# Optimization experiments

Hardware: AMD Instinct MI355X
Metric: run time of the kernel (lower is better)

The kernel has to match this reference:

```python
import jax, jax.numpy as jnp
import numpy as np


def hard_sigmoid(x):
    # Keras hard_sigmoid: clip(0.2*x + 0.5, 0, 1)
    return jnp.clip(0.2 * x + 0.5, 0.0, 1.0)


def setup_inputs() -> dict:
    key = jax.random.key(0)
    k1, k2, k3 = jax.random.split(key, 3)
    B, H, W, C = 32, 64, 64, 256
    x = jax.random.normal(k1, (B, H, W, C), dtype=jnp.float32)
    # glorot_uniform over (C, W, H): fan_in = W (last-two matmul dims are W x H)
    limit = np.sqrt(6.0 / (W + H)).astype(np.float32)
    Wq = jax.random.uniform(k2, (C, W, H), minval=-limit, maxval=limit, dtype=jnp.float32)
    Wk = jax.random.uniform(k3, (C, W, H), minval=-limit, maxval=limit, dtype=jnp.float32)
    return {"x": x, "Wq": Wq, "Wk": Wk}


def reference(x, Wq, Wk):
    # x: [B, H, W, C] -> [B, C, H, W]
    xt = jnp.transpose(x, (0, 3, 1, 2))
    # projections: [B,C,H,W] @ [C,W,H] (broadcast over B) -> [B,C,H,H]
    q = hard_sigmoid(jnp.einsum('bchw,cwk->bchk', xt, Wq))
    K = jnp.tanh(jnp.einsum('bchw,cwk->bchk', xt, Wk))
    # scores: q @ K^T over last two dims -> [B,C,H,H]
    qk = hard_sigmoid(jnp.einsum('bchk,bcmk->bchm', q, K))
    qk = jax.nn.softmax(qk, axis=-1)
    # output: [B,C,H,W] @ [B,C,W(==H),H] -> [B,C,H,H]
    out = jnp.einsum('bchw,bcwm->bchm', xt, qk)
    # back to channels-last [B,H,W,C]
    return jnp.transpose(out, (0, 2, 3, 1))
```

## Files before the change

### kernel.cpp

```cpp
#include <hip/hip_runtime.h>
#include <hip/hip_bf16.h>


typedef short short8 __attribute__((ext_vector_type(8)));
typedef float floatx4 __attribute__((ext_vector_type(4)));
typedef unsigned int uint;

#define PW 16896
#define BUF1_OFF 8192

__device__ __forceinline__ uint bfr(float f) {
  uint u = __float_as_uint(f);
  return (u + 0x7FFFu + ((u >> 16) & 1u)) >> 16;
}
__device__ __forceinline__ uint pk2(float a, float b) {
  return bfr(a) | (bfr(b) << 16);
}
__device__ __forceinline__ short8 u4s8(uint a, uint b, uint c, uint d) {
  union { uint u[4]; short8 s; } t;
  t.u[0] = a; t.u[1] = b; t.u[2] = c; t.u[3] = d;
  return t.s;
}
__device__ __forceinline__ float hsg(float x) {
  return fminf(fmaxf(0.2f * x + 0.5f, 0.f), 1.f);
}

__global__ __launch_bounds__(256, 2) void fused_attn(
    const float* __restrict__ x, const float* __restrict__ Wq,
    const float* __restrict__ Wk, float* __restrict__ out) {
  __shared__ __align__(16) unsigned char smem[4 * PW];

  const int tid  = threadIdx.x;
  const int lane = tid & 63;
  const int wid  = tid >> 6;
  const int l15  = lane & 15;
  const int quad = lane >> 4;

  const int b  = blockIdx.x & 31;
  const int cg = blockIdx.x >> 5;
  const int c0 = cg << 2;
  const int c  = c0 + wid;

  unsigned char* buf0 = smem + wid * PW;
  unsigned char* buf1 = buf0 + BUF1_OFF;

  {
    const float* xb = x + (size_t)b * 4096 * 256 + c0;
#pragma unroll 4
    for (int it = 0; it < 16; ++it) {
      int hw = it * 256 + tid;
      float4 v = *(const float4*)(xb + (size_t)hw * 256);
      int h = hw >> 6, w = hw & 63;
      uint off = (uint)(h * 128 + (((w >> 3) ^ (h & 7)) << 4) + ((w & 7) << 1));
      float vv[4] = {v.x, v.y, v.z, v.w};
#pragma unroll
      for (int j = 0; j < 4; ++j)
        *(unsigned short*)(smem + j * PW + off) = (unsigned short)bfr(vv[j]);
    }
  }
  __syncthreads();

  short8 xf[4][2];
#pragma unroll
  for (int rt = 0; rt < 4; ++rt) {
    int r = rt * 16 + l15;
#pragma unroll
    for (int ks = 0; ks < 2; ++ks)
      xf[rt][ks] = *(const short8*)(buf0 + r * 128 + ((((ks * 4 + quad) ^ (r & 7))) << 4));
  }

  const floatx4 zero4 = {0.f, 0.f, 0.f, 0.f};
  floatx4 acc[16];

  {
    const float* wp = Wq + (size_t)c * 4096;
#pragma unroll 4
    for (int j = 0; j < 16; ++j) {
      int f4 = j * 64 + lane;
      float4 v = *(const float4*)(wp + (size_t)f4 * 4);
      int w = f4 >> 4, k0 = (f4 & 15) << 2;
      uint2 pk; pk.x = pk2(v.x, v.y); pk.y = pk2(v.z, v.w);
      *(uint2*)(buf1 + w * 136 + k0 * 2) = pk;
    }
  }
#pragma unroll
  for (int i = 0; i < 16; ++i) acc[i] = zero4;
#pragma unroll
  for (int kt = 0; kt < 4; ++kt) {
    short8 af[2];
#pragma unroll
    for (int ks = 0; ks < 2; ++ks) {
      const unsigned short* p = (const unsigned short*)buf1 + (ks * 32 + quad * 8) * 68 + (kt * 16 + l15);
      af[ks] = u4s8((uint)p[0]   | ((uint)p[68]  << 16),
                    (uint)p[136] | ((uint)p[204] << 16),
                    (uint)p[272] | ((uint)p[340] << 16),
                    (uint)p[408] | ((uint)p[476] << 16));
    }
#pragma unroll
    for (int ht = 0; ht < 4; ++ht) {
      acc[kt * 4 + ht] = __builtin_amdgcn_mfma_f32_16x16x32_bf16(af[0], xf[ht][0], acc[kt * 4 + ht], 0, 0, 0);
      acc[kt * 4 + ht] = __builtin_amdgcn_mfma_f32_16x16x32_bf16(af[1], xf[ht][1], acc[kt * 4 + ht], 0, 0, 0);
    }
  }
#pragma unroll
  for (int kt = 0; kt < 4; ++kt)
#pragma unroll
    for (int ht = 0; ht < 4; ++ht) {
      floatx4 a = acc[kt * 4 + ht];
      uint2 pk; pk.x = pk2(hsg(a[0]), hsg(a[1])); pk.y = pk2(hsg(a[2]), hsg(a[3]));
      int h = ht * 16 + l15;
      *(uint2*)(buf0 + h * 128 + ((((kt * 2 + (quad >> 1)) ^ (h & 7))) << 4) + ((quad & 1) << 3)) = pk;
    }

  {
    const float* wp = Wk + (size_t)c * 4096;
#pragma unroll 4
    for (int j = 0; j < 16; ++j) {
      int f4 = j * 64 + lane;
      float4 v = *(const float4*)(wp + (size_t)f4 * 4);
      int w = f4 >> 4, k0 = (f4 & 15) << 2;
      uint2 pk; pk.x = pk2(v.x, v.y); pk.y = pk2(v.z, v.w);
      *(uint2*)(buf1 + w * 136 + k0 * 2) = pk;
    }
  }
#pragma unroll
  for (int i = 0; i < 16; ++i) acc[i] = zero4;
#pragma unroll
  for (int kt = 0; kt < 4; ++kt) {
    short8 af[2];
#pragma unroll
    for (int ks = 0; ks < 2; ++ks) {
      const unsigned short* p = (const unsigned short*)buf1 + (ks * 32 + quad * 8) * 68 + (kt * 16 + l15);
      af[ks] = u4s8((uint)p[0]   | ((uint)p[68]  << 16),
                    (uint)p[136] | ((uint)p[204] << 16),
                    (uint)p[272] | ((uint)p[340] << 16),
                    (uint)p[408] | ((uint)p[476] << 16));
    }
#pragma unroll
    for (int ht = 0; ht < 4; ++ht) {
      acc[kt * 4 + ht] = __builtin_amdgcn_mfma_f32_16x16x32_bf16(af[0], xf[ht][0], acc[kt * 4 + ht], 0, 0, 0);
      acc[kt * 4 + ht] = __builtin_amdgcn_mfma_f32_16x16x32_bf16(af[1], xf[ht][1], acc[kt * 4 + ht], 0, 0, 0);
    }
  }
#pragma unroll
  for (int kt = 0; kt < 4; ++kt)
#pragma unroll
    for (int ht = 0; ht < 4; ++ht) {
      floatx4 a = acc[kt * 4 + ht];
      float kv[4];
#pragma unroll
      for (int i = 0; i < 4; ++i) {
        float t = __expf(2.f * a[i]);
        kv[i] = 1.f - 2.f / (t + 1.f);
      }
      uint2 pk; pk.x = pk2(kv[0], kv[1]); pk.y = pk2(kv[2], kv[3]);
      int m = ht * 16 + l15;
      *(uint2*)(buf1 + m * 128 + ((((kt * 2 + (quad >> 1)) ^ (m & 7))) << 4) + ((quad & 1) << 3)) = pk;
    }

  short8 kf[4][2];
#pragma unroll
  for (int mt = 0; mt < 4; ++mt) {
    int r = mt * 16 + l15;
#pragma unroll
    for (int ks = 0; ks < 2; ++ks)
      kf[mt][ks] = *(const short8*)(buf1 + r * 128 + ((((ks * 4 + quad) ^ (r & 7))) << 4));
  }
#pragma unroll
  for (int i = 0; i < 16; ++i) acc[i] = zero4;
#pragma unroll
  for (int wt = 0; wt < 4; ++wt) {
    int r = wt * 16 + l15;
    short8 qf0 = *(const short8*)(buf0 + r * 128 + (((quad ^ (r & 7))) << 4));
    short8 qf1 = *(const short8*)(buf0 + r * 128 + ((((4 + quad) ^ (r & 7))) << 4));
#pragma unroll
    for (int mt = 0; mt < 4; ++mt) {
      acc[wt * 4 + mt] = __builtin_amdgcn_mfma_f32_16x16x32_bf16(qf0, kf[mt][0], acc[wt * 4 + mt], 0, 0, 0);
      acc[wt * 4 + mt] = __builtin_amdgcn_mfma_f32_16x16x32_bf16(qf1, kf[mt][1], acc[wt * 4 + mt], 0, 0, 0);
    }
  }
#pragma unroll
  for (int i = 0; i < 16; ++i)
#pragma unroll
    for (int j = 0; j < 4; ++j) acc[i][j] = __expf(hsg(acc[i][j]));
  float inv[4][4];
#pragma unroll
  for (int wt = 0; wt < 4; ++wt)
#pragma unroll
    for (int i = 0; i < 4; ++i) {
      float p = acc[wt * 4 + 0][i] + acc[wt * 4 + 1][i] + acc[wt * 4 + 2][i] + acc[wt * 4 + 3][i];
      p += __shfl_xor(p, 1, 16);
      p += __shfl_xor(p, 2, 16);
      p += __shfl_xor(p, 4, 16);
      p += __shfl_xor(p, 8, 16);
      inv[wt][i] = 1.f / p;
    }
#pragma unroll
  for (int wt = 0; wt < 4; ++wt)
#pragma unroll
    for (int mt = 0; mt < 4; ++mt) {
      floatx4 a = acc[wt * 4 + mt];
      uint2 pk;
      pk.x = pk2(a[0] * inv[wt][0], a[1] * inv[wt][1]);
      pk.y = pk2(a[2] * inv[wt][2], a[3] * inv[wt][3]);
      int m = mt * 16 + l15;
      *(uint2*)(buf0 + m * 128 + ((((wt * 2 + (quad >> 1)) ^ (m & 7))) << 4) + ((quad & 1) << 3)) = pk;
    }

#pragma unroll
  for (int i = 0; i < 16; ++i) acc[i] = zero4;
#pragma unroll
  for (int mt = 0; mt < 4; ++mt) {
    int r = mt * 16 + l15;
    short8 sf0 = *(const short8*)(buf0 + r * 128 + (((quad ^ (r & 7))) << 4));
    short8 sf1 = *(const short8*)(buf0 + r * 128 + ((((4 + quad) ^ (r & 7))) << 4));
#pragma unroll
    for (int ht = 0; ht < 4; ++ht) {
      acc[mt * 4 + ht] = __builtin_amdgcn_mfma_f32_16x16x32_bf16(sf0, xf[ht][0], acc[mt * 4 + ht], 0, 0, 0);
      acc[mt * 4 + ht] = __builtin_amdgcn_mfma_f32_16x16x32_bf16(sf1, xf[ht][1], acc[mt * 4 + ht], 0, 0, 0);
    }
  }
#pragma unroll
  for (int mt = 0; mt < 4; ++mt)
#pragma unroll
    for (int ht = 0; ht < 4; ++ht) {
      floatx4 a = acc[mt * 4 + ht];
      uint2 pk; pk.x = pk2(a[0], a[1]); pk.y = pk2(a[2], a[3]);
      int h = ht * 16 + l15;
      *(uint2*)(buf1 + h * 128 + ((((mt * 2 + (quad >> 1)) ^ (h & 7))) << 4) + ((quad & 1) << 3)) = pk;
    }
  __syncthreads();

  const size_t outbase = (size_t)b * 4096 * 256 + c0;
#pragma unroll
  for (int rep = 0; rep < 4; ++rep) {
    int idx = rep * 256 + tid;
    int h = idx >> 4, mq = idx & 15;
    uint loff = (uint)(h * 128 + ((((mq >> 1) ^ (h & 7))) << 4) + ((mq & 1) << 3));
    float vals[4][4];
#pragma unroll
    for (int j = 0; j < 4; ++j) {
      uint2 d = *(const uint2*)(smem + j * PW + BUF1_OFF + loff);
      vals[j][0] = __uint_as_float(d.x << 16);
      vals[j][1] = __uint_as_float(d.x & 0xFFFF0000u);
      vals[j][2] = __uint_as_float(d.y << 16);
      vals[j][3] = __uint_as_float(d.y & 0xFFFF0000u);
    }
    float* op = out + outbase + (size_t)(h * 64 + mq * 4) * 256;
#pragma unroll
    for (int jj = 0; jj < 4; ++jj) {
      float4 v = {vals[0][jj], vals[1][jj], vals[2][jj], vals[3][jj]};
      *(float4*)(op + (size_t)jj * 256) = v;
    }
  }
}

extern "C" void kernel_launch(void* const* d_in, const int* in_sizes, int n_in,
                              void* d_out, int out_size, void* d_ws, size_t ws_size,
                              hipStream_t stream) {
  const float* x  = (const float*)d_in[0];
  const float* Wq = (const float*)d_in[1];
  const float* Wk = (const float*)d_in[2];
  float* o = (float*)d_out;
  fused_attn<<<dim3(2048), dim3(256), 0, stream>>>(x, Wq, Wk, o);
}
```

Measured before the change: 323.7 us.

## Prepack weights in prep kernel, use register lane swaps and hardware bf16 convert

Adds a prep kernel that converts Wq/Wk to bf16 once, already laid out as MFMA A-operand fragments in workspace. The main kernel no longer reloads and transposes the weights per batch block. Q and the softmax scores are rearranged into MFMA operand layout with permlane swaps in registers instead of a round trip through LDS, which shrinks LDS use enough to target 3 blocks per CU. It also switches bf16 rounding to the v_cvt_pk_bf16_f32 instruction, widens the x loads, and wraps MFMA loops in s_setprio. The risks are an extra kernel launch and higher register pressure from holding fragments in registers.

Result: slower. 332.8 us (+2.8%).

```diff
diff --git a/kernel.cpp b/kernel.cpp
--- a/kernel.cpp
+++ b/kernel.cpp
@@ -1,20 +1,14 @@
 #include <hip/hip_runtime.h>
-#include <hip/hip_bf16.h>
 
 
 typedef short short8 __attribute__((ext_vector_type(8)));
 typedef float floatx4 __attribute__((ext_vector_type(4)));
 typedef unsigned int uint;
 
-#define PW 16896
-#define BUF1_OFF 8192
-
-__device__ __forceinline__ uint bfr(float f) {
-  uint u = __float_as_uint(f);
-  return (u + 0x7FFFu + ((u >> 16) & 1u)) >> 16;
-}
-__device__ __forceinline__ uint pk2(float a, float b) {
-  return bfr(a) | (bfr(b) << 16);
+__device__ __forceinline__ uint cvtpk(float a, float b) {
+  uint r;
+  asm("v_cvt_pk_bf16_f32 %0, %1, %2" : "=v"(r) : "v"(a), "v"(b));
+  return r;
 }
 __device__ __forceinline__ short8 u4s8(uint a, uint b, uint c, uint d) {
   union { uint u[4]; short8 s; } t;
@@ -25,10 +19,74 @@
   return fminf(fmaxf(0.2f * x + 0.5f, 0.f), 1.f);
 }
 
-__global__ __launch_bounds__(256, 2) void fused_attn(
-    const float* __restrict__ x, const float* __restrict__ Wq,
-    const float* __restrict__ Wk, float* __restrict__ out) {
-  __shared__ __align__(16) unsigned char smem[4 * PW];
+__device__ __forceinline__ void pl32swap(uint A, uint C, uint& lo, uint& hi, int quad) {
+#if __has_builtin(__builtin_amdgcn_permlane32_swap)
+  auto r = __builtin_amdgcn_permlane32_swap(A, C, false, false);
+  lo = (uint)r[0]; hi = (uint)r[1];
+#else
+  uint sA = __shfl_xor(A, 32), sC = __shfl_xor(C, 32);
+  bool up = quad >= 2;
+  lo = up ? sC : A;
+  hi = up ? C : sA;
+#endif
+}
+__device__ __forceinline__ void pl16swap(uint A, uint C, uint& lo, uint& hi, int quad) {
+#if __has_builtin(__builtin_amdgcn_permlane16_swap)
+  auto r = __builtin_amdgcn_permlane16_swap(A, C, false, false);
+  lo = (uint)r[0]; hi = (uint)r[1];
+#else
+  uint sA = (uint)__builtin_amdgcn_ds_swizzle((int)A, 0x401F);
+  uint sC = (uint)__builtin_amdgcn_ds_swizzle((int)C, 0x401F);
+  bool odd = quad & 1;
+  lo = odd ? sC : A;
+  hi = odd ? C : sA;
+#endif
+}
+__device__ __forceinline__ short8 xchg4(uint A, uint B, uint C, uint D, int quad) {
+  uint Ap, Cp, Bp, Dp, t0, t1, t2, t3;
+  pl32swap(A, C, Ap, Cp, quad);
+  pl32swap(B, D, Bp, Dp, quad);
+  pl16swap(Ap, Cp, t0, t2, quad);
+  pl16swap(Bp, Dp, t1, t3, quad);
+  return u4s8(t0, t1, t2, t3);
+}
+
+__global__ __launch_bounds__(256) void prep_w(const float* __restrict__ Wq,
+                                              const float* __restrict__ Wk,
+                                              unsigned short* __restrict__ ws) {
+  __shared__ __align__(16) unsigned char sm[4 * 8704];
+  const int tid = threadIdx.x, lane = tid & 63, wid = tid >> 6;
+  const int task = blockIdx.x * 4 + wid;
+  const int c = task & 255;
+  const float* wp = ((task >> 8) ? Wk : Wq) + (size_t)c * 4096;
+  unsigned char* buf = sm + wid * 8704;
+  const int l15 = lane & 15, quad = lane >> 4;
+#pragma unroll 4
+  for (int j = 0; j < 16; ++j) {
+    int f4 = j * 64 + lane;
+    float4 v = *(const float4*)(wp + (size_t)f4 * 4);
+    int w = f4 >> 4, k0 = (f4 & 15) << 2;
+    uint2 pk; pk.x = cvtpk(v.x, v.y); pk.y = cvtpk(v.z, v.w);
+    *(uint2*)(buf + w * 136 + k0 * 2) = pk;
+  }
+  unsigned short* dst = ws + (size_t)task * 4096;
+#pragma unroll
+  for (int kt = 0; kt < 4; ++kt)
+#pragma unroll
+    for (int ks = 0; ks < 2; ++ks) {
+      const unsigned short* p = (const unsigned short*)buf + (ks * 32 + quad * 8) * 68 + (kt * 16 + l15);
+      short8 af = u4s8((uint)p[0]   | ((uint)p[68]  << 16),
+                       (uint)p[136] | ((uint)p[204] << 16),
+                       (uint)p[272] | ((uint)p[340] << 16),
+                       (uint)p[408] | ((uint)p[476] << 16));
+      *(short8*)(dst + ((kt * 2 + ks) * 64 + lane) * 8) = af;
+    }
+}
+
+__global__ __launch_bounds__(256, 3) void fused_attn(
+    const float* __restrict__ x, const unsigned short* __restrict__ wsp,
+    float* __restrict__ out) {
+  __shared__ __align__(16) unsigned char smem[4 * 8192];
 
   const int tid  = threadIdx.x;
   const int lane = tid & 63;
@@ -41,21 +99,33 @@
   const int c0 = cg << 2;
   const int c  = c0 + wid;
 
-  unsigned char* buf0 = smem + wid * PW;
-  unsigned char* buf1 = buf0 + BUF1_OFF;
+  unsigned char* buf0 = smem + wid * 8192;
+
+  const short8* wqf = (const short8*)wsp + (size_t)c * 512;
+  const short8* wkf = wqf + 256 * 512;
+
+  short8 aq[4][2];
+#pragma unroll
+  for (int kt = 0; kt < 4; ++kt)
+#pragma unroll
+    for (int ks = 0; ks < 2; ++ks) aq[kt][ks] = wqf[(kt * 2 + ks) * 64 + lane];
 
   {
     const float* xb = x + (size_t)b * 4096 * 256 + c0;
-#pragma unroll 4
-    for (int it = 0; it < 16; ++it) {
-      int hw = it * 256 + tid;
-      float4 v = *(const float4*)(xb + (size_t)hw * 256);
-      int h = hw >> 6, w = hw & 63;
-      uint off = (uint)(h * 128 + (((w >> 3) ^ (h & 7)) << 4) + ((w & 7) << 1));
-      float vv[4] = {v.x, v.y, v.z, v.w};
-#pragma unroll
-      for (int j = 0; j < 4; ++j)
-        *(unsigned short*)(smem + j * PW + off) = (unsigned short)bfr(vv[j]);
+#pragma unroll
+    for (int i = 0; i < 8; ++i) {
+      int p = i * 256 + tid;
+      int h = p >> 5, w0 = (p & 31) << 1;
+      const float* src = xb + (size_t)(h * 64 + w0) * 256;
+      float4 v0 = *(const float4*)src;
+      float4 v1 = *(const float4*)(src + 256);
+      uint off = (uint)(h * 128 + (((w0 >> 3) ^ (h & 7)) << 4) + ((w0 & 7) << 1));
+      uint pw0 = cvtpk(v0.x, v1.x), pw1 = cvtpk(v0.y, v1.y);
+      uint pw2 = cvtpk(v0.z, v1.z), pw3 = cvtpk(v0.w, v1.w);
+      *(uint*)(smem + 0 * 8192 + off) = pw0;
+      *(uint*)(smem + 1 * 8192 + off) = pw1;
+      *(uint*)(smem + 2 * 8192 + off) = pw2;
+      *(uint*)(smem + 3 * 8192 + off) = pw3;
     }
   }
   __syncthreads();
@@ -66,81 +136,52 @@
     int r = rt * 16 + l15;
 #pragma unroll
     for (int ks = 0; ks < 2; ++ks)
-      xf[rt][ks] = *(const short8*)(buf0 + r * 128 + ((((ks * 4 + quad) ^ (r & 7))) << 4));
+      xf[rt][ks] = *(const short8*)(buf0 + r * 128 + (((ks * 4 + quad) ^ (r & 7)) << 4));
   }
 
   const floatx4 zero4 = {0.f, 0.f, 0.f, 0.f};
   floatx4 acc[16];
 
-  {
-    const float* wp = Wq + (size_t)c * 4096;
-#pragma unroll 4
-    for (int j = 0; j < 16; ++j) {
-      int f4 = j * 64 + lane;
-      float4 v = *(const float4*)(wp + (size_t)f4 * 4);
-      int w = f4 >> 4, k0 = (f4 & 15) << 2;
-      uint2 pk; pk.x = pk2(v.x, v.y); pk.y = pk2(v.z, v.w);
-      *(uint2*)(buf1 + w * 136 + k0 * 2) = pk;
-    }
-  }
 #pragma unroll
   for (int i = 0; i < 16; ++i) acc[i] = zero4;
+  __builtin_amdgcn_s_setprio(1);
+#pragma unroll
+  for (int kt = 0; kt < 4; ++kt)
+#pragma unroll
+    for (int ht = 0; ht < 4; ++ht) {
+      acc[kt * 4 + ht] = __builtin_amdgcn_mfma_f32_16x16x32_bf16(aq[kt][0], xf[ht][0], acc[kt * 4 + ht], 0, 0, 0);
+      acc[kt * 4 + ht] = __builtin_amdgcn_mfma_f32_16x16x32_bf16(aq[kt][1], xf[ht][1], acc[kt * 4 + ht], 0, 0, 0);
+    }
+  __builtin_amdgcn_s_setprio(0);
+
+  short8 qf[4][2];
+#pragma unroll
+  for (int ht = 0; ht < 4; ++ht) {
+    uint s[4][2];
+#pragma unroll
+    for (int kt = 0; kt < 4; ++kt) {
+      floatx4 a = acc[kt * 4 + ht];
+      s[kt][0] = cvtpk(hsg(a[0]), hsg(a[1]));
+      s[kt][1] = cvtpk(hsg(a[2]), hsg(a[3]));
+    }
+#pragma unroll
+    for (int ks = 0; ks < 2; ++ks)
+      qf[ht][ks] = xchg4(s[2 * ks][0], s[2 * ks][1], s[2 * ks + 1][0], s[2 * ks + 1][1], quad);
+  }
+
+#pragma unroll
+  for (int i = 0; i < 16; ++i) acc[i] = zero4;
 #pragma unroll
   for (int kt = 0; kt < 4; ++kt) {
-    short8 af[2];
-#pragma unroll
-    for (int ks = 0; ks < 2; ++ks) {
-      const unsigned short* p = (const unsigned short*)buf1 + (ks * 32 + quad * 8) * 68 + (kt * 16 + l15);
-      af[ks] = u4s8((uint)p[0]   | ((uint)p[68]  << 16),
-                    (uint)p[136] | ((uint)p[204] << 16),
-                    (uint)p[272] | ((uint)p[340] << 16),
-                    (uint)p[408] | ((uint)p[476] << 16));
-    }
-#pragma unroll
-    for (int ht = 0; ht < 4; ++ht) {
-      acc[kt * 4 + ht] = __builtin_amdgcn_mfma_f32_16x16x32_bf16(af[0], xf[ht][0], acc[kt * 4 + ht], 0, 0, 0);
-      acc[kt * 4 + ht] = __builtin_amdgcn_mfma_f32_16x16x32_bf16(af[1], xf[ht][1], acc[kt * 4 + ht], 0, 0, 0);
-    }
-  }
-#pragma unroll
-  for (int kt = 0; kt < 4; ++kt)
-#pragma unroll
-    for (int ht = 0; ht < 4; ++ht) {
-      floatx4 a = acc[kt * 4 + ht];
-      uint2 pk; pk.x = pk2(hsg(a[0]), hsg(a[1])); pk.y = pk2(hsg(a[2]), hsg(a[3]));
-      int h = ht * 16 + l15;
-      *(uint2*)(buf0 + h * 128 + ((((kt * 2 + (quad >> 1)) ^ (h & 7))) << 4) + ((quad & 1) << 3)) = pk;
-    }
-
-  {
-    const float* wp = Wk + (size_t)c * 4096;
-#pragma unroll 4
-    for (int j = 0; j < 16; ++j) {
-      int f4 = j * 64 + lane;
-      float4 v = *(const float4*)(wp + (size_t)f4 * 4);
-      int w = f4 >> 4, k0 = (f4 & 15) << 2;
-      uint2 pk; pk.x = pk2(v.x, v.y); pk.y = pk2(v.z, v.w);
-      *(uint2*)(buf1 + w * 136 + k0 * 2) = pk;
-    }
-  }
-#pragma unroll
-  for (int i = 0; i < 16; ++i) acc[i] = zero4;
-#pragma unroll
-  for (int kt = 0; kt < 4; ++kt) {
-    short8 af[2];
-#pragma unroll
-    for (int ks = 0; ks < 2; ++ks) {
-      const unsigned short* p = (const unsigned short*)buf1 + (ks * 32 + quad * 8) * 68 + (kt * 16 + l15);
-      af[ks] = u4s8((uint)p[0]   | ((uint)p[68]  << 16),
-                    (uint)p[136] | ((uint)p[204] << 16),
-                    (uint)p[272] | ((uint)p[340] << 16),
-                    (uint)p[408] | ((uint)p[476] << 16));
-    }
-#pragma unroll
-    for (int ht = 0; ht < 4; ++ht) {
-      acc[kt * 4 + ht] = __builtin_amdgcn_mfma_f32_16x16x32_bf16(af[0], xf[ht][0], acc[kt * 4 + ht], 0, 0, 0);
-      acc[kt * 4 + ht] = __builtin_amdgcn_mfma_f32_16x16x32_bf16(af[1], xf[ht][1], acc[kt * 4 + ht], 0, 0, 0);
-    }
+    short8 a0 = wkf[(kt * 2 + 0) * 64 + lane];
+    short8 a1 = wkf[(kt * 2 + 1) * 64 + lane];
+    __builtin_amdgcn_s_setprio(1);
+#pragma unroll
+    for (int ht = 0; ht < 4; ++ht) {
+      acc[kt * 4 + ht] = __builtin_amdgcn_mfma_f32_16x16x32_bf16(a0, xf[ht][0], acc[kt * 4 + ht], 0, 0, 0);
+      acc[kt * 4 + ht] = __builtin_amdgcn_mfma_f32_16x16x32_bf16(a1, xf[ht][1], acc[kt * 4 + ht], 0, 0, 0);
+    }
+    __builtin_amdgcn_s_setprio(0);
   }
 #pragma unroll
   for (int kt = 0; kt < 4; ++kt)
@@ -153,31 +194,25 @@
         float t = __expf(2.f * a[i]);
         kv[i] = 1.f - 2.f / (t + 1.f);
       }
-      uint2 pk; pk.x = pk2(kv[0], kv[1]); pk.y = pk2(kv[2], kv[3]);
+      uint2 pk; pk.x = cvtpk(kv[0], kv[1]); pk.y = cvtpk(kv[2], kv[3]);
       int m = ht * 16 + l15;
-      *(uint2*)(buf1 + m * 128 + ((((kt * 2 + (quad >> 1)) ^ (m & 7))) << 4) + ((quad & 1) << 3)) = pk;
-    }
-
-  short8 kf[4][2];
+      *(uint2*)(buf0 + m * 128 + ((((kt * 2 + (quad >> 1)) ^ (m & 7))) << 4) + ((quad & 1) << 3)) = pk;
+    }
+
+#pragma unroll
+  for (int i = 0; i < 16; ++i) acc[i] = zero4;
 #pragma unroll
   for (int mt = 0; mt < 4; ++mt) {
     int r = mt * 16 + l15;
-#pragma unroll
-    for (int ks = 0; ks < 2; ++ks)
-      kf[mt][ks] = *(const short8*)(buf1 + r * 128 + ((((ks * 4 + quad) ^ (r & 7))) << 4));
-  }
-#pragma unroll
-  for (int i = 0; i < 16; ++i) acc[i] = zero4;
-#pragma unroll
-  for (int wt = 0; wt < 4; ++wt) {
-    int r = wt * 16 + l15;
-    short8 qf0 = *(const short8*)(buf0 + r * 128 + (((quad ^ (r & 7))) << 4));
-    short8 qf1 = *(const short8*)(buf0 + r * 128 + ((((4 + quad) ^ (r & 7))) << 4));
-#pragma unroll
-    for (int mt = 0; mt < 4; ++mt) {
-      acc[wt * 4 + mt] = __builtin_amdgcn_mfma_f32_16x16x32_bf16(qf0, kf[mt][0], acc[wt * 4 + mt], 0, 0, 0);
-      acc[wt * 4 + mt] = __builtin_amdgcn_mfma_f32_16x16x32_bf16(qf1, kf[mt][1], acc[wt * 4 + mt], 0, 0, 0);
-    }
+    short8 kf0 = *(const short8*)(buf0 + r * 128 + (((quad) ^ (r & 7)) << 4));
+    short8 kf1 = *(const short8*)(buf0 + r * 128 + (((4 + quad) ^ (r & 7)) << 4));
+    __builtin_amdgcn_s_setprio(1);
+#pragma unroll
+    for (int wt = 0; wt < 4; ++wt) {
+      acc[wt * 4 + mt] = __builtin_amdgcn_mfma_f32_16x16x32_bf16(qf[wt][0], kf0, acc[wt * 4 + mt], 0, 0, 0);
+      acc[wt * 4 + mt] = __builtin_amdgcn_mfma_f32_16x16x32_bf16(qf[wt][1], kf1, acc[wt * 4 + mt], 0, 0, 0);
+    }
+    __builtin_amdgcn_s_setprio(0);
   }
 #pragma unroll
   for (int i = 0; i < 16; ++i)
@@ -195,39 +230,40 @@
       p += __shfl_xor(p, 8, 16);
       inv[wt][i] = 1.f / p;
     }
-#pragma unroll
-  for (int wt = 0; wt < 4; ++wt)
-#pragma unroll
-    for (int mt = 0; mt < 4; ++mt) {
+  short8 sf[4][2];
+#pragma unroll
+  for (int mt = 0; mt < 4; ++mt) {
+    uint s[4][2];
+#pragma unroll
+    for (int wt = 0; wt < 4; ++wt) {
       floatx4 a = acc[wt * 4 + mt];
-      uint2 pk;
-      pk.x = pk2(a[0] * inv[wt][0], a[1] * inv[wt][1]);
-      pk.y = pk2(a[2] * inv[wt][2], a[3] * inv[wt][3]);
-      int m = mt * 16 + l15;
-      *(uint2*)(buf0 + m * 128 + ((((wt * 2 + (quad >> 1)) ^ (m & 7))) << 4) + ((quad & 1) << 3)) = pk;
-    }
+      s[wt][0] = cvtpk(a[0] * inv[wt][0], a[1] * inv[wt][1]);
+      s[wt][1] = cvtpk(a[2] * inv[wt][2], a[3] * inv[wt][3]);
+    }
+#pragma unroll
+    for (int ks = 0; ks < 2; ++ks)
+      sf[mt][ks] = xchg4(s[2 * ks][0], s[2 * ks][1], s[2 * ks + 1][0], s[2 * ks + 1][1], quad);
+  }
 
 #pragma unroll
   for (int i = 0; i < 16; ++i) acc[i] = zero4;
-#pragma unroll
-  for (int mt = 0; mt < 4; ++mt) {
-    int r = mt * 16 + l15;
-    short8 sf0 = *(const short8*)(buf0 + r * 128 + (((quad ^ (r & 7))) << 4));
-    short8 sf1 = *(const short8*)(buf0 + r * 128 + ((((4 + quad) ^ (r & 7))) << 4));
-#pragma unroll
-    for (int ht = 0; ht < 4; ++ht) {
-      acc[mt * 4 + ht] = __builtin_amdgcn_mfma_f32_16x16x32_bf16(sf0, xf[ht][0], acc[mt * 4 + ht], 0, 0, 0);
-      acc[mt * 4 + ht] = __builtin_amdgcn_mfma_f32_16x16x32_bf16(sf1, xf[ht][1], acc[mt * 4 + ht], 0, 0, 0);
-    }
-  }
+  __builtin_amdgcn_s_setprio(1);
 #pragma unroll
   for (int mt = 0; mt < 4; ++mt)
 #pragma unroll
     for (int ht = 0; ht < 4; ++ht) {
+      acc[mt * 4 + ht] = __builtin_amdgcn_mfma_f32_16x16x32_bf16(sf[mt][0], xf[ht][0], acc[mt * 4 + ht], 0, 0, 0);
+      acc[mt * 4 + ht] = __builtin_amdgcn_mfma_f32_16x16x32_bf16(sf[mt][1], xf[ht][1], acc[mt * 4 + ht], 0, 0, 0);
+    }
+  __builtin_amdgcn_s_setprio(0);
+#pragma unroll
+  for (int mt = 0; mt < 4; ++mt)
+#pragma unroll
+    for (int ht = 0; ht < 4; ++ht) {
       floatx4 a = acc[mt * 4 + ht];
-      uint2 pk; pk.x = pk2(a[0], a[1]); pk.y = pk2(a[2], a[3]);
+      uint2 pk; pk.x = cvtpk(a[0], a[1]); pk.y = cvtpk(a[2], a[3]);
       int h = ht * 16 + l15;
-      *(uint2*)(buf1 + h * 128 + ((((mt * 2 + (quad >> 1)) ^ (h & 7))) << 4) + ((quad & 1) << 3)) = pk;
+      *(uint2*)(buf0 + h * 128 + ((((mt * 2 + (quad >> 1)) ^ (h & 7))) << 4) + ((quad & 1) << 3)) = pk;
     }
   __syncthreads();
 
@@ -240,7 +276,7 @@
     float vals[4][4];
 #pragma unroll
     for (int j = 0; j < 4; ++j) {
-      uint2 d = *(const uint2*)(smem + j * PW + BUF1_OFF + loff);
+      uint2 d = *(const uint2*)(smem + j * 8192 + loff);
       vals[j][0] = __uint_as_float(d.x << 16);
       vals[j][1] = __uint_as_float(d.x & 0xFFFF0000u);
       vals[j][2] = __uint_as_float(d.y << 16);
@@ -261,6 +297,7 @@
   const float* x  = (const float*)d_in[0];
   const float* Wq = (const float*)d_in[1];
   const float* Wk = (const float*)d_in[2];
-  float* o = (float*)d_out;
-  fused_attn<<<dim3(2048), dim3(256), 0, stream>>>(x, Wq, Wk, o);
-}
+  unsigned short* ws = (unsigned short*)d_ws;
+  prep_w<<<dim3(128), dim3(256), 0, stream>>>(Wq, Wk, ws);
+  fused_attn<<<dim3(2048), dim3(256), 0, stream>>>(x, ws, (float*)d_out);
+}
```
